# Kernel tuning notes

Measured on AMD Instinct MI355X. Metric: run time of the kernel, lower is better.

The kernel has to match this reference:

```python
import jax, jax.numpy as jnp
from jax import lax
import numpy as np

B, T, F_IN = 64, 3072, 128
CONV_OUT, K, STRIDE = 64, 3, 3
HID, OUT = 256, 10


def setup_inputs() -> dict:
    key = jax.random.key(0)
    ks = jax.random.split(key, 10)
    s = 0.05
    return {
        "input": jax.random.normal(ks[0], (B, T, F_IN), jnp.float32),
        "r": jnp.zeros(((T - K) // STRIDE + 1, B, CONV_OUT), jnp.float32),
        "hx0": jax.random.normal(ks[1], (B, HID), jnp.float32),
        "cx0": jax.random.normal(ks[2], (B, HID), jnp.float32),
        "conv_w": jax.random.normal(ks[3], (CONV_OUT, F_IN, K), jnp.float32) * s,
        "conv_b": jnp.zeros((CONV_OUT,), jnp.float32),
        "w_ih": jax.random.normal(ks[4], (4 * HID, CONV_OUT), jnp.float32) * s,
        "b_ih": jnp.zeros((4 * HID,), jnp.float32),
        "w_hh": jax.random.normal(ks[5], (4 * HID, HID), jnp.float32) * s,
        "b_hh": jnp.zeros((4 * HID,), jnp.float32),
        "lin_w": jax.random.normal(ks[6], (OUT, HID), jnp.float32) * s,
        "lin_b": jnp.zeros((OUT,), jnp.float32),
        "batch_size": B,
    }


def reference(input, r, hx0, cx0, conv_w, conv_b, w_ih, b_ih, w_hh, b_hh, lin_w, lin_b, batch_size):
    # F.normalize: L2 normalize along dim=1 (the time dim), eps=1e-12
    norm = jnp.sqrt(jnp.sum(input * input, axis=1, keepdims=True))
    x = input / jnp.maximum(norm, 1e-12)
    x = jnp.transpose(x, (0, 2, 1))  # [B, F_IN, T]
    x = lax.conv_general_dilated(
        x, conv_w, window_strides=(STRIDE,), padding='VALID',
        dimension_numbers=('NCH', 'OIH', 'NCH')) + conv_b[None, :, None]
    x = jax.nn.relu(x)
    x = jnp.transpose(x, (2, 0, 1))  # [T', B, 64]

    def step(carry, xt):
        h, c = carry
        gates = xt @ w_ih.T + b_ih + h @ w_hh.T + b_hh  # [B, 4H]
        i, f, g, o = jnp.split(gates, 4, axis=-1)
        c = jax.nn.sigmoid(f) * c + jax.nn.sigmoid(i) * jnp.tanh(g)
        h = jax.nn.sigmoid(o) * jnp.tanh(c)
        return (h, c), None

    (h, _), _ = lax.scan(step, (hx0, cx0), x)
    return h @ lin_w.T + lin_b  # [B, OUT]
```

## Files before the change

kernel.cpp:

```cpp
#include <hip/hip_runtime.h>
#include <math.h>

#define B_N 64
#define T_N 3072
#define FIN 128
#define TP 1024
#define COUT 64
#define HID 256
#define G4 1024
#define OUT_N 10
#define NCHUNK 24
#define CHUNK_T (T_N / NCHUNK)

#define WREG 24
#define WLDS 8

typedef _Float16 h2_t __attribute__((ext_vector_type(2)));
typedef unsigned u32x4 __attribute__((ext_vector_type(4)));

#if defined(__has_builtin)
#if __has_builtin(__builtin_amdgcn_fdot2)
#define HAVE_FDOT2 1
#endif
#endif

__device__ __forceinline__ float fdot2(unsigned w, unsigned h, float acc) {
#ifdef HAVE_FDOT2
    return __builtin_amdgcn_fdot2(__builtin_bit_cast(h2_t, w),
                                  __builtin_bit_cast(h2_t, h), acc, false);
#else
    h2_t wv = __builtin_bit_cast(h2_t, w), hv = __builtin_bit_cast(h2_t, h);
    return acc + (float)wv.x * (float)hv.x + (float)wv.y * (float)hv.y;
#endif
}

__device__ __forceinline__ unsigned pack2(float a, float b) {
    unsigned la = (unsigned)__builtin_bit_cast(unsigned short, (_Float16)a);
    unsigned lb = (unsigned)__builtin_bit_cast(unsigned short, (_Float16)b);
    return la | (lb << 16);
}

__device__ __forceinline__ int gperm(int c) {
    int sub = (c >> 9) & 1;
    int cc  = c & 511;
    int slot = (cc < 256) ? (cc << 1) : (((cc - 256) << 1) | 1);
    return slot | (sub << 9);
}

__device__ __forceinline__ float swap1(float x) {
    int i = __builtin_bit_cast(int, x);
#if defined(__has_builtin)
#if __has_builtin(__builtin_amdgcn_mov_dpp)
    int r = __builtin_amdgcn_mov_dpp(i, 0xB1, 0xF, 0xF, true);
#else
    int r = __shfl_xor(i, 1, 64);
#endif
#else
    int r = __shfl_xor(i, 1, 64);
#endif
    return __builtin_bit_cast(float, r);
}

__global__ void pack_weights(const float* __restrict__ w_ih,
                             const float* __restrict__ w_hh,
                             unsigned* __restrict__ whhR,
                             unsigned* __restrict__ whhL,
                             float* __restrict__ wihT) {
    int col = blockIdx.x, d = threadIdx.x;
    int pcol = gperm(col);
    const float* wr = w_hh + col * HID;
    unsigned p = pack2(wr[2 * d], wr[2 * d + 1]);
    int c = d >> 2, r = d & 3;
    if (c < WREG) whhR[(c * 1024 + pcol) * 4 + r] = p;
    else          whhL[((c - WREG) * 1024 + pcol) * 4 + r] = p;
    if (d < COUT) wihT[d * 1024 + col] = w_ih[col * COUT + d];
}

__global__ void prep_conv_w(const float* __restrict__ conv_w, float* __restrict__ wc2) {
    int i = blockIdx.x * 256 + threadIdx.x;
    if (i < 24576) {
        int j = i >> 6, oc = i & 63;
        int kk = j >> 7, ic = j & 127;
        wc2[i] = conv_w[(oc * 128 + ic) * 3 + kk];
    }
}

__global__ void norm_partial(const float* __restrict__ in, float* __restrict__ part) {
    int b = blockIdx.x, ch = blockIdx.y, f = threadIdx.x;
    const float* p = in + ((size_t)b * T_N + (size_t)ch * CHUNK_T) * FIN + f;
    float s0 = 0.f, s1 = 0.f, s2 = 0.f, s3 = 0.f;
#pragma unroll
    for (int r = 0; r < CHUNK_T; r += 4) {
        float v0 = p[(r + 0) * FIN];
        float v1 = p[(r + 1) * FIN];
        float v2 = p[(r + 2) * FIN];
        float v3 = p[(r + 3) * FIN];
        s0 += v0 * v0; s1 += v1 * v1; s2 += v2 * v2; s3 += v3 * v3;
    }
    part[(b * NCHUNK + ch) * FIN + f] = (s0 + s1) + (s2 + s3);
}

__global__ __launch_bounds__(256) void conv_relu(
        const float* __restrict__ in, const float* __restrict__ part,
        const float* __restrict__ wc2, const float* __restrict__ cb,
        float* __restrict__ X) {
    __shared__ __align__(16) float xs[16 * 384];
    __shared__ __align__(16) float wsh[96 * 64];
    __shared__ float invn[FIN];

    int b = blockIdx.x, tile = blockIdx.y;
    int tid = threadIdx.x;

    if (tid < FIN) {
        float s = 0.f;
#pragma unroll
        for (int c = 0; c < NCHUNK; c++) s += part[(b * NCHUNK + c) * FIN + tid];
        invn[tid] = rsqrtf(fmaxf(s, 1e-24f));
    }
    __syncthreads();

    const float* ip = in + ((size_t)b * T_N + (size_t)tile * 48) * FIN;
    for (int i = tid; i < 6144; i += 256) xs[i] = ip[i] * invn[i & 127];

    int oc = tid & 63, tq = tid >> 6;
    float acc0 = 0.f, acc1 = 0.f, acc2 = 0.f, acc3 = 0.f;
    const float* xb = xs + tq * 4 * 384;

    for (int c = 0; c < 4; c++) {
        __syncthreads();
        for (int i = tid; i < 6144; i += 256) wsh[i] = wc2[c * 6144 + i];
        __syncthreads();
#pragma unroll 8
        for (int jj = 0; jj < 96; jj += 4) {
            int j = c * 96 + jj;
            float w0 = wsh[(jj + 0) * 64 + oc];
            float w1 = wsh[(jj + 1) * 64 + oc];
            float w2 = wsh[(jj + 2) * 64 + oc];
            float w3 = wsh[(jj + 3) * 64 + oc];
            float4 x0 = *(const float4*)(xb + j);
            float4 x1 = *(const float4*)(xb + 384 + j);
            float4 x2 = *(const float4*)(xb + 768 + j);
            float4 x3 = *(const float4*)(xb + 1152 + j);
            acc0 += w0 * x0.x + w1 * x0.y + w2 * x0.z + w3 * x0.w;
            acc1 += w0 * x1.x + w1 * x1.y + w2 * x1.z + w3 * x1.w;
            acc2 += w0 * x2.x + w1 * x2.y + w2 * x2.z + w3 * x2.w;
            acc3 += w0 * x3.x + w1 * x3.y + w2 * x3.z + w3 * x3.w;
        }
    }
    float bb = cb[oc];
    int tp0 = tile * 16 + tq * 4;
    size_t o = ((size_t)b * TP + tp0) * COUT + oc;
    X[o]       = fmaxf(acc0 + bb, 0.f);
    X[o + 64]  = fmaxf(acc1 + bb, 0.f);
    X[o + 128] = fmaxf(acc2 + bb, 0.f);
    X[o + 192] = fmaxf(acc3 + bb, 0.f);
}

__global__ __launch_bounds__(256) void x_gemm(
        const float* __restrict__ X, const float* __restrict__ wihT,
        const float* __restrict__ b_ih, const float* __restrict__ b_hh,
        _Float16* __restrict__ xg) {
    __shared__ float xs[64 * 17];
    int b = blockIdx.x, t0 = blockIdx.y * 16, tid = threadIdx.x;

    const float* Xp = X + ((size_t)b * TP + t0) * COUT;
    for (int i = tid; i < 1024; i += 256) {
        int r = i >> 6, k = i & 63;
        xs[k * 17 + r] = Xp[i];
    }
    __syncthreads();

    unsigned* xgu = (unsigned*)xg;
#pragma unroll
    for (int half = 0; half < 2; half++) {
        int cA = half * 512 + tid;
        int cB = cA + 256;
        float bA = b_ih[cA] + b_hh[cA];
        float bB = b_ih[cB] + b_hh[cB];
        float accA[16], accB[16];
#pragma unroll
        for (int r = 0; r < 16; r++) { accA[r] = bA; accB[r] = bB; }
        for (int k = 0; k < 64; k++) {
            float wA = wihT[k * 1024 + cA];
            float wB = wihT[k * 1024 + cB];
#pragma unroll
            for (int r = 0; r < 16; r++) {
                float xv = xs[k * 17 + r];
                accA[r] += wA * xv;
                accB[r] += wB * xv;
            }
        }
#pragma unroll
        for (int r = 0; r < 16; r++)
            xgu[((size_t)b * TP + t0 + r) * 512 + half * 256 + tid] =
                pack2(accA[r], accB[r]);
    }
}

__device__ __forceinline__ float fsig(float x) {
    return 1.f / (1.f + __expf(-x));
}
__device__ __forceinline__ float ftanh(float x) {
    float xc = fminf(fmaxf(x, -15.f), 15.f);
    float e = __expf(2.f * xc);
    return (e - 1.f) / (e + 1.f);
}

#define SM_WL   0
#define SM_H    131072
#define SM_H32  132096
#define SM_SIZE 133120

#define REP24(M) M(0) M(1) M(2) M(3) M(4) M(5) M(6) M(7) M(8) M(9) M(10) M(11) \
                 M(12) M(13) M(14) M(15) M(16) M(17) M(18) M(19) M(20) M(21) M(22) M(23)
#define REP8(M)  M(0) M(1) M(2) M(3) M(4) M(5) M(6) M(7)

#define DECLW(n)  u32x4 wa##n, wb##n;
#define LOADW(n)  wa##n = whhR4[(n) * 1024 + j]; wb##n = whhR4[(n) * 1024 + j + 512];

#define DOTCH(n)  { \
    unsigned h0 = (unsigned)__builtin_amdgcn_readlane((int)hvv.x, 2 * (n)); \
    unsigned h1 = (unsigned)__builtin_amdgcn_readlane((int)hvv.y, 2 * (n)); \
    unsigned h2 = (unsigned)__builtin_amdgcn_readlane((int)hvv.x, 2 * (n) + 1); \
    unsigned h3 = (unsigned)__builtin_amdgcn_readlane((int)hvv.y, 2 * (n) + 1); \
    a0 = fdot2(wa##n[0], h0, a0); a1 = fdot2(wb##n[0], h0, a1); \
    a0 = fdot2(wa##n[1], h1, a0); a1 = fdot2(wb##n[1], h1, a1); \
    a0 = fdot2(wa##n[2], h2, a0); a1 = fdot2(wb##n[2], h2, a1); \
    a0 = fdot2(wa##n[3], h3, a0); a1 = fdot2(wb##n[3], h3, a1); }

#define DOTLDS(m) { u32x4 WA = wL[(m) * 1024 + j]; u32x4 WB = wL[(m) * 1024 + j + 512]; \
    unsigned h0 = (unsigned)__builtin_amdgcn_readlane((int)hvv.x, 2 * (WREG + (m))); \
    unsigned h1 = (unsigned)__builtin_amdgcn_readlane((int)hvv.y, 2 * (WREG + (m))); \
    unsigned h2 = (unsigned)__builtin_amdgcn_readlane((int)hvv.x, 2 * (WREG + (m)) + 1); \
    unsigned h3 = (unsigned)__builtin_amdgcn_readlane((int)hvv.y, 2 * (WREG + (m)) + 1); \
    a0 = fdot2(WA[0], h0, a0); a1 = fdot2(WB[0], h0, a1); \
    a0 = fdot2(WA[1], h1, a0); a1 = fdot2(WB[1], h1, a1); \
    a0 = fdot2(WA[2], h2, a0); a1 = fdot2(WB[2], h2, a1); \
    a0 = fdot2(WA[3], h3, a0); a1 = fdot2(WB[3], h3, a1); }

__global__ __attribute__((amdgpu_flat_work_group_size(512, 512),
                          amdgpu_waves_per_eu(2, 2)))
void lstm_kernel(
        const u32x4* __restrict__ whhR4, const u32x4* __restrict__ whhL4,
        const _Float16* __restrict__ xg,
        const float* __restrict__ hx0, const float* __restrict__ cx0,
        const float* __restrict__ lin_w, const float* __restrict__ lin_b,
        float* __restrict__ out) {
    extern __shared__ char smem[];
    u32x4*    wL    = (u32x4*)(smem + SM_WL);
    _Float16* hbuf  = (_Float16*)(smem + SM_H);
    float*    h32_s = (float*)(smem + SM_H32);

    const int b = blockIdx.x, j = threadIdx.x;
    const int lane = j & 63;
    const int m = j >> 1;
    const int odd = j & 1;

    REP24(DECLW)
    REP24(LOADW)

    for (int i = j; i < WLDS * 1024; i += 512) wL[i] = whhL4[i];

    float c_reg = 0.f;
    if (odd) c_reg = cx0[b * HID + m];
    if (j < HID) hbuf[j] = (_Float16)hx0[b * HID + j];

    const _Float16* Xg = xg + (size_t)b * TP * G4;
    _Float16 xa = Xg[j], xb = Xg[j + 512];
    __syncthreads();

    for (int t = 0; t < TP; t++) {
        const uint2* hp = (const uint2*)(hbuf + (t & 1) * 256);
        uint2 hvv = hp[lane];

        _Float16 xan = (_Float16)0.f, xbn = (_Float16)0.f;
        if (t + 1 < TP) {
            xan = Xg[(t + 1) * G4 + j];
            xbn = Xg[(t + 1) * G4 + j + 512];
        }

        float a0 = (float)xa, a1 = (float)xb;
        REP24(DOTCH)
        REP8(DOTLDS)

        float sa = fsig(a0);
        float p  = sa * ftanh(a1);
        float pn = swap1(p);
        if (odd) {
            float so = fsig(a1);
            c_reg = sa * c_reg + pn;
            float hh = so * ftanh(c_reg);
            hbuf[((t + 1) & 1) * 256 + m] = (_Float16)hh;
            if (t == TP - 1) h32_s[m] = hh;
        }
        __syncthreads();
        xa = xan; xb = xbn;
    }

    if (j < OUT_N) {
        float s = lin_b[j];
        const float* lw = lin_w + j * HID;
#pragma unroll 4
        for (int k = 0; k < HID; k++) s += h32_s[k] * lw[k];
        out[b * OUT_N + j] = s;
    }
}

extern "C" void kernel_launch(void* const* d_in, const int* in_sizes, int n_in,
                              void* d_out, int out_size, void* d_ws, size_t ws_size,
                              hipStream_t stream) {
    const float* input  = (const float*)d_in[0];
    const float* hx0    = (const float*)d_in[2];
    const float* cx0    = (const float*)d_in[3];
    const float* conv_w = (const float*)d_in[4];
    const float* conv_b = (const float*)d_in[5];
    const float* w_ih   = (const float*)d_in[6];
    const float* b_ih   = (const float*)d_in[7];
    const float* w_hh   = (const float*)d_in[8];
    const float* b_hh   = (const float*)d_in[9];
    const float* lin_w  = (const float*)d_in[10];
    const float* lin_b  = (const float*)d_in[11];

    float* ws = (float*)d_ws;
    float*     part = ws;
    float*     X    = part + 196608;
    float*     wc2  = X + 4194304;
    float*     wihT = wc2 + 24576;
    unsigned*  whhR = (unsigned*)(wihT + 65536);
    unsigned*  whhL = whhR + WREG * 1024 * 4;
    _Float16*  xg   = (_Float16*)(whhL + WLDS * 1024 * 4);

    (void)hipFuncSetAttribute((const void*)lstm_kernel,
                              hipFuncAttributeMaxDynamicSharedMemorySize, SM_SIZE);

    pack_weights<<<1024, 128, 0, stream>>>(w_ih, w_hh, whhR, whhL, wihT);
    prep_conv_w<<<96, 256, 0, stream>>>(conv_w, wc2);
    norm_partial<<<dim3(B_N, NCHUNK), FIN, 0, stream>>>(input, part);
    conv_relu<<<dim3(B_N, 64), 256, 0, stream>>>(input, part, wc2, conv_b, X);
    x_gemm<<<dim3(B_N, 64), 256, 0, stream>>>(X, wihT, b_ih, b_hh, xg);
    lstm_kernel<<<B_N, 512, SM_SIZE, stream>>>(
        (const u32x4*)whhR, (const u32x4*)whhL, xg,
        hx0, cx0, lin_w, lin_b, (float*)d_out);
}
```

Baseline: 2.594 ms.

## Pin recurrent weights in AGPRs, vectorize x_gemm, and make the prefetch branchless

The recurrent weights held in registers are now written explicitly into accumulation registers (AGPRs) with inline asm and read back into VGPRs each step. This frees VGPR pressure and avoids spills. The input-projection GEMM is restructured so each thread computes all four gates at once using float4 LDS reads (padded stride 20) instead of two half passes. The next-step input prefetch is made unconditional by clamping the index. The AGPR reads add one extra instruction per weight per timestep on the serial critical path, and the volatile asm may hinder scheduling.

```diff
diff --git a/kernel.cpp b/kernel.cpp
--- a/kernel.cpp
+++ b/kernel.cpp
@@ -17,6 +17,7 @@
 
 typedef _Float16 h2_t __attribute__((ext_vector_type(2)));
 typedef unsigned u32x4 __attribute__((ext_vector_type(4)));
+typedef float    f32x4 __attribute__((ext_vector_type(4)));
 
 #if defined(__has_builtin)
 #if __has_builtin(__builtin_amdgcn_fdot2)
@@ -160,40 +161,51 @@
         const float* __restrict__ X, const float* __restrict__ wihT,
         const float* __restrict__ b_ih, const float* __restrict__ b_hh,
         _Float16* __restrict__ xg) {
-    __shared__ float xs[64 * 17];
+    __shared__ __align__(16) float xs[64 * 20];
     int b = blockIdx.x, t0 = blockIdx.y * 16, tid = threadIdx.x;
 
     const float* Xp = X + ((size_t)b * TP + t0) * COUT;
     for (int i = tid; i < 1024; i += 256) {
         int r = i >> 6, k = i & 63;
-        xs[k * 17 + r] = Xp[i];
+        xs[k * 20 + r] = Xp[i];
     }
     __syncthreads();
 
+    int cI = tid, cF = tid + 256, cG = tid + 512, cO = tid + 768;
+    float bI = b_ih[cI] + b_hh[cI];
+    float bF = b_ih[cF] + b_hh[cF];
+    float bG = b_ih[cG] + b_hh[cG];
+    float bO = b_ih[cO] + b_hh[cO];
+
+    f32x4 aI[4], aF[4], aG[4], aO[4];
+#pragma unroll
+    for (int q = 0; q < 4; q++) {
+        aI[q] = bI; aF[q] = bF; aG[q] = bG; aO[q] = bO;
+    }
+
+    for (int k = 0; k < 64; k++) {
+        float wI = wihT[k * 1024 + cI];
+        float wF = wihT[k * 1024 + cF];
+        float wG = wihT[k * 1024 + cG];
+        float wO = wihT[k * 1024 + cO];
+        const f32x4* xv = (const f32x4*)(xs + k * 20);
+#pragma unroll
+        for (int q = 0; q < 4; q++) {
+            f32x4 x4 = xv[q];
+            aI[q] += wI * x4;
+            aF[q] += wF * x4;
+            aG[q] += wG * x4;
+            aO[q] += wO * x4;
+        }
+    }
+
     unsigned* xgu = (unsigned*)xg;
-#pragma unroll
-    for (int half = 0; half < 2; half++) {
-        int cA = half * 512 + tid;
-        int cB = cA + 256;
-        float bA = b_ih[cA] + b_hh[cA];
-        float bB = b_ih[cB] + b_hh[cB];
-        float accA[16], accB[16];
-#pragma unroll
-        for (int r = 0; r < 16; r++) { accA[r] = bA; accB[r] = bB; }
-        for (int k = 0; k < 64; k++) {
-            float wA = wihT[k * 1024 + cA];
-            float wB = wihT[k * 1024 + cB];
-#pragma unroll
-            for (int r = 0; r < 16; r++) {
-                float xv = xs[k * 17 + r];
-                accA[r] += wA * xv;
-                accB[r] += wB * xv;
-            }
-        }
-#pragma unroll
-        for (int r = 0; r < 16; r++)
-            xgu[((size_t)b * TP + t0 + r) * 512 + half * 256 + tid] =
-                pack2(accA[r], accB[r]);
+    size_t base = ((size_t)b * TP + t0) * 512;
+#pragma unroll
+    for (int r = 0; r < 16; r++) {
+        int q = r >> 2, e = r & 3;
+        xgu[base + (size_t)r * 512 + tid]       = pack2(aI[q][e], aF[q][e]);
+        xgu[base + (size_t)r * 512 + 256 + tid] = pack2(aG[q][e], aO[q][e]);
     }
 }
 
@@ -215,18 +227,38 @@
                  M(12) M(13) M(14) M(15) M(16) M(17) M(18) M(19) M(20) M(21) M(22) M(23)
 #define REP8(M)  M(0) M(1) M(2) M(3) M(4) M(5) M(6) M(7)
 
-#define DECLW(n)  u32x4 wa##n, wb##n;
-#define LOADW(n)  wa##n = whhR4[(n) * 1024 + j]; wb##n = whhR4[(n) * 1024 + j + 512];
+#define DECLW(n)  unsigned wa##n##_0, wa##n##_1, wa##n##_2, wa##n##_3, \
+                           wb##n##_0, wb##n##_1, wb##n##_2, wb##n##_3;
+
+#define LOADW(n)  { u32x4 t = whhR4[(n) * 1024 + j]; \
+    asm volatile("v_accvgpr_write_b32 %0, %1" : "=a"(wa##n##_0) : "v"(t[0])); \
+    asm volatile("v_accvgpr_write_b32 %0, %1" : "=a"(wa##n##_1) : "v"(t[1])); \
+    asm volatile("v_accvgpr_write_b32 %0, %1" : "=a"(wa##n##_2) : "v"(t[2])); \
+    asm volatile("v_accvgpr_write_b32 %0, %1" : "=a"(wa##n##_3) : "v"(t[3])); \
+    t = whhR4[(n) * 1024 + j + 512]; \
+    asm volatile("v_accvgpr_write_b32 %0, %1" : "=a"(wb##n##_0) : "v"(t[0])); \
+    asm volatile("v_accvgpr_write_b32 %0, %1" : "=a"(wb##n##_1) : "v"(t[1])); \
+    asm volatile("v_accvgpr_write_b32 %0, %1" : "=a"(wb##n##_2) : "v"(t[2])); \
+    asm volatile("v_accvgpr_write_b32 %0, %1" : "=a"(wb##n##_3) : "v"(t[3])); }
 
 #define DOTCH(n)  { \
+    unsigned A0, A1, A2, A3, B0, B1, B2, B3; \
+    asm volatile("v_accvgpr_read_b32 %0, %1" : "=v"(A0) : "a"(wa##n##_0)); \
+    asm volatile("v_accvgpr_read_b32 %0, %1" : "=v"(B0) : "a"(wb##n##_0)); \
+    asm volatile("v_accvgpr_read_b32 %0, %1" : "=v"(A1) : "a"(wa##n##_1)); \
+    asm volatile("v_accvgpr_read_b32 %0, %1" : "=v"(B1) : "a"(wb##n##_1)); \
+    asm volatile("v_accvgpr_read_b32 %0, %1" : "=v"(A2) : "a"(wa##n##_2)); \
+    asm volatile("v_accvgpr_read_b32 %0, %1" : "=v"(B2) : "a"(wb##n##_2)); \
+    asm volatile("v_accvgpr_read_b32 %0, %1" : "=v"(A3) : "a"(wa##n##_3)); \
+    asm volatile("v_accvgpr_read_b32 %0, %1" : "=v"(B3) : "a"(wb##n##_3)); \
     unsigned h0 = (unsigned)__builtin_amdgcn_readlane((int)hvv.x, 2 * (n)); \
     unsigned h1 = (unsigned)__builtin_amdgcn_readlane((int)hvv.y, 2 * (n)); \
     unsigned h2 = (unsigned)__builtin_amdgcn_readlane((int)hvv.x, 2 * (n) + 1); \
     unsigned h3 = (unsigned)__builtin_amdgcn_readlane((int)hvv.y, 2 * (n) + 1); \
-    a0 = fdot2(wa##n[0], h0, a0); a1 = fdot2(wb##n[0], h0, a1); \
-    a0 = fdot2(wa##n[1], h1, a0); a1 = fdot2(wb##n[1], h1, a1); \
-    a0 = fdot2(wa##n[2], h2, a0); a1 = fdot2(wb##n[2], h2, a1); \
-    a0 = fdot2(wa##n[3], h3, a0); a1 = fdot2(wb##n[3], h3, a1); }
+    a0 = fdot2(A0, h0, a0); a1 = fdot2(B0, h0, a1); \
+    a0 = fdot2(A1, h1, a0); a1 = fdot2(B1, h1, a1); \
+    a0 = fdot2(A2, h2, a0); a1 = fdot2(B2, h2, a1); \
+    a0 = fdot2(A3, h3, a0); a1 = fdot2(B3, h3, a1); }
 
 #define DOTLDS(m) { u32x4 WA = wL[(m) * 1024 + j]; u32x4 WB = wL[(m) * 1024 + j + 512]; \
     unsigned h0 = (unsigned)__builtin_amdgcn_readlane((int)hvv.x, 2 * (WREG + (m))); \
@@ -273,11 +305,9 @@
         const uint2* hp = (const uint2*)(hbuf + (t & 1) * 256);
         uint2 hvv = hp[lane];
 
-        _Float16 xan = (_Float16)0.f, xbn = (_Float16)0.f;
-        if (t + 1 < TP) {
-            xan = Xg[(t + 1) * G4 + j];
-            xbn = Xg[(t + 1) * G4 + j + 512];
-        }
+        int tn = (t + 1 < TP) ? t + 1 : t;
+        _Float16 xan = Xg[(size_t)tn * G4 + j];
+        _Float16 xbn = Xg[(size_t)tn * G4 + j + 512];
 
         float a0 = (float)xa, a1 = (float)xb;
         REP24(DOTCH)
```

New measurement: 3.246 ms. +25.1%, slower.
